# Optimization experiments

Hardware: AMD Instinct MI355X
Metric: run time of the kernel (lower is better)

## Reference

```python
import jax, jax.numpy as jnp
import numpy as np

N_NODES = 50000
N_EDGES = 800000
D_FEAT = 128
D_HID = 500


def setup_inputs() -> dict:
    key = jax.random.key(0)
    k1, k2, k3, k4 = jax.random.split(key, 4)
    x = jax.random.normal(k1, (N_NODES, D_FEAT), dtype=jnp.float32)
    edge_index = jax.random.randint(k2, (2, N_EDGES), 0, N_NODES, dtype=jnp.int64)
    # Glorot-ish init for weights, zeros for bias (PyG GCNConv default)
    W1 = jax.random.normal(k3, (D_FEAT, D_HID), dtype=jnp.float32) / np.sqrt(D_FEAT)
    b1 = jnp.zeros((D_HID,), dtype=jnp.float32)
    W2 = jax.random.normal(k4, (D_HID, 1), dtype=jnp.float32) / np.sqrt(D_HID)
    b2 = jnp.zeros((1,), dtype=jnp.float32)
    return {"x": x, "edge_index": edge_index, "W1": W1, "b1": b1, "W2": W2, "b2": b2}


def gcn_conv(x, W, b, src, dst, n_nodes):
    """PyG GCNConv: linear transform, add self-loops, symmetric norm, scatter-add, bias."""
    h = x @ W  # [N, out]
    loops = jnp.arange(n_nodes, dtype=src.dtype)
    s = jnp.concatenate([src, loops])  # [E+N]
    d = jnp.concatenate([dst, loops])
    deg = jnp.zeros((n_nodes,), dtype=h.dtype).at[d].add(1.0)
    dinv = jnp.where(deg > 0, jax.lax.rsqrt(deg), 0.0)
    norm = dinv[s] * dinv[d]  # [E+N]
    msg = h[s] * norm[:, None]  # [E+N, out] -- dominant memory traffic
    out = jax.ops.segment_sum(msg, d, num_segments=n_nodes)
    return out + b


def reference(x, edge_index, W1, b1, W2, b2):
    src, dst = edge_index[0], edge_index[1]
    n = x.shape[0]
    h = gcn_conv(x, W1, b1, src, dst, n)
    h = jax.nn.relu(h)
    # F.dropout(training=self.training): identity in eval mode
    out = gcn_conv(h, W2, b2, src, dst, n)
    return out
```

## Files before the change

### kernel.cpp

```cpp
#include <hip/hip_runtime.h>


#define N_NODES 50000
#define N_EDGES 800000
#define D_FEAT  128
#define D_HID   500
#define NTILES  3125
#define RB      782
#define CSTRIDE 64

typedef __bf16 bf16x8 __attribute__((ext_vector_type(8)));
typedef float  f32x4  __attribute__((ext_vector_type(4)));

static __device__ inline unsigned int f2bf(float f) {
    unsigned int u = __float_as_uint(f);
    return (u + 0x7fffu + ((u >> 16) & 1u)) >> 16;
}
static __device__ inline float bf_lo(unsigned int u) { return __uint_as_float(u << 16); }
static __device__ inline float bf_hi(unsigned int u) { return __uint_as_float(u & 0xffff0000u); }

static __device__ inline void add8(float* acc, uint4 u) {
    acc[0] += bf_lo(u.x);
    acc[1] += bf_hi(u.x);
    acc[2] += bf_lo(u.y);
    acc[3] += bf_hi(u.y);
    acc[4] += bf_lo(u.z);
    acc[5] += bf_hi(u.z);
    acc[6] += bf_lo(u.w);
    acc[7] += bf_hi(u.w);
}

__global__ __launch_bounds__(256) void k_rank(const int* __restrict__ dst,
                                              const float* __restrict__ W1,
                                              const float* __restrict__ b1,
                                              const float* __restrict__ W2,
                                              int* __restrict__ deg,
                                              int* __restrict__ rank,
                                              unsigned short* __restrict__ b_pk,
                                              float* __restrict__ b1p,
                                              float* __restrict__ w2p) {
    const int b = blockIdx.x, tid = threadIdx.x;
    if (b < RB) {
        int t4 = b * 256 + tid;
        if (t4 < N_EDGES / 4) {
            int e = t4 * 4;
            int4 d4 = *(const int4*)&dst[e];
            int4 r4;
            r4.x = atomicAdd(&deg[d4.x], 1);
            r4.y = atomicAdd(&deg[d4.y], 1);
            r4.z = atomicAdd(&deg[d4.z], 1);
            r4.w = atomicAdd(&deg[d4.w], 1);
            *(int4*)&rank[e] = r4;
        }
    } else if (b < RB + 32) {
        int idx  = (b - RB) * 256 + tid;
        int lane = idx & 63;
        int slot = idx >> 6;
        int t    = slot >> 2;
        int ks   = slot & 3;
        int quad = lane >> 4;
        int n    = t * 16 + (lane & 15);
        unsigned int us[8];
#pragma unroll
        for (int j = 0; j < 8; j++) {
            int k = ks * 32 + quad * 8 + j;
            float v = (n < D_HID) ? W1[(size_t)k * D_HID + n] : 0.f;
            us[j] = f2bf(v);
        }
        uint4 p;
        p.x = us[0] | (us[1] << 16);
        p.y = us[2] | (us[3] << 16);
        p.z = us[4] | (us[5] << 16);
        p.w = us[6] | (us[7] << 16);
        ((uint4*)b_pk)[idx] = p;
    } else {
        for (int i = tid; i < 512; i += 256) {
            b1p[i] = (i < D_HID) ? b1[i] : 0.f;
            w2p[i] = (i < D_HID) ? W2[i] : 0.f;
        }
    }
}

__global__ __launch_bounds__(256) void k_fill(const int* __restrict__ src,
                                              const int* __restrict__ dst,
                                              const int* __restrict__ rank,
                                              const int* __restrict__ deg,
                                              const float* __restrict__ x,
                                              int* __restrict__ csrp,
                                              uint2* __restrict__ xd) {
    const int e = blockIdx.x * 256 + threadIdx.x;
    {
        int r = rank[e];
        if (r < CSTRIDE)
            csrp[dst[e] * CSTRIDE + r] = src[e];
    }
    for (int i = e; i < N_NODES * D_FEAT / 4; i += N_EDGES) {
        float d = rsqrtf((float)(deg[i >> 5] + 1));
        float4 v = ((const float4*)x)[i];
        uint2 o;
        o.x = f2bf(d * v.x) | (f2bf(d * v.y) << 16);
        o.y = f2bf(d * v.z) | (f2bf(d * v.w) << 16);
        xd[i] = o;
    }
}

__global__ __launch_bounds__(256, 4) void k_gcn1(const uint4* __restrict__ xd4,
                                                 const int* __restrict__ csrp,
                                                 const int* __restrict__ deg,
                                                 const unsigned short* __restrict__ b_pk,
                                                 const float* __restrict__ b1p,
                                                 const float* __restrict__ w2p,
                                                 float* __restrict__ zd) {
    __shared__ unsigned short A[16][136];
    __shared__ float red[4][16];
    const int t = threadIdx.x;
    const int node0 = blockIdx.x * 16;
    const int wv = t >> 6, lane = t & 63;
    const int q = lane >> 4, p = lane & 15;

    {
        const int n = wv * 4 + q;
        const int node = node0 + n;
        int dg = deg[node];
        if (dg > CSTRIDE) dg = CSTRIDE;
        const int base = node * CSTRIDE;
        float acc[8];
#pragma unroll
        for (int j = 0; j < 8; j++) acc[j] = 0.f;

        int e = 0;
        for (; e + 4 <= dg; e += 4) {
            int4 s4 = *(const int4*)&csrp[base + e];
            uint4 u0 = xd4[(size_t)s4.x * 16 + p];
            uint4 u1 = xd4[(size_t)s4.y * 16 + p];
            uint4 u2 = xd4[(size_t)s4.z * 16 + p];
            uint4 u3 = xd4[(size_t)s4.w * 16 + p];
            add8(acc, u0);
            add8(acc, u1);
            add8(acc, u2);
            add8(acc, u3);
        }
        for (; e < dg; e++) {
            int s = csrp[base + e];
            uint4 u = xd4[(size_t)s * 16 + p];
            add8(acc, u);
        }

        const float di = rsqrtf((float)(dg + 1));
        uint4 su = xd4[(size_t)node * 16 + p];
        uint4 o;
        o.x = f2bf(di * (acc[0] + bf_lo(su.x))) |
              (f2bf(di * (acc[1] + bf_hi(su.x))) << 16);
        o.y = f2bf(di * (acc[2] + bf_lo(su.y))) |
              (f2bf(di * (acc[3] + bf_hi(su.y))) << 16);
        o.z = f2bf(di * (acc[4] + bf_lo(su.z))) |
              (f2bf(di * (acc[5] + bf_hi(su.z))) << 16);
        o.w = f2bf(di * (acc[6] + bf_lo(su.w))) |
              (f2bf(di * (acc[7] + bf_hi(su.w))) << 16);
        *(uint4*)&A[n][p * 8] = o;
    }
    __syncthreads();

    bf16x8 afr[4];
#pragma unroll
    for (int ks = 0; ks < 4; ks++)
        afr[ks] = *(const bf16x8*)&A[p][ks * 32 + q * 8];

    const bf16x8* __restrict__ bpk = (const bf16x8*)b_pk;
    f32x4 acc[8];
#pragma unroll
    for (int tt = 0; tt < 8; tt++) acc[tt] = (f32x4){0.f, 0.f, 0.f, 0.f};
#pragma unroll
    for (int tt = 0; tt < 8; tt++) {
        const int tile_n = wv * 8 + tt;
#pragma unroll
        for (int ks = 0; ks < 4; ks++) {
            bf16x8 bfr = bpk[(size_t)(tile_n * 4 + ks) * 64 + lane];
            acc[tt] = __builtin_amdgcn_mfma_f32_16x16x32_bf16(afr[ks], bfr, acc[tt], 0, 0, 0);
        }
    }

    float zp[4] = {0.f, 0.f, 0.f, 0.f};
#pragma unroll
    for (int tt = 0; tt < 8; tt++) {
        const int c = (wv * 8 + tt) * 16 + p;
        const float b1v = b1p[c];
        const float w2v = w2p[c];
#pragma unroll
        for (int r = 0; r < 4; r++)
            zp[r] += fmaxf(acc[tt][r] + b1v, 0.f) * w2v;
    }
#pragma unroll
    for (int off = 1; off < 16; off <<= 1) {
#pragma unroll
        for (int r = 0; r < 4; r++) zp[r] += __shfl_xor(zp[r], off);
    }
    if (p == 0) {
#pragma unroll
        for (int r = 0; r < 4; r++) red[wv][q * 4 + r] = zp[r];
    }
    __syncthreads();
    if (t < 16) {
        int node = node0 + t;
        float zz = red[0][t] + red[1][t] + red[2][t] + red[3][t];
        zd[node] = rsqrtf((float)(deg[node] + 1)) * zz;
    }
}

__global__ __launch_bounds__(256) void k_gz(const int* __restrict__ csrp,
                                            const int* __restrict__ deg,
                                            const float* __restrict__ zd,
                                            const float* __restrict__ b2,
                                            float* __restrict__ out) {
    const int node = blockIdx.x * 16 + (threadIdx.x >> 4);
    const int l = threadIdx.x & 15;
    int dg = deg[node];
    if (dg > CSTRIDE) dg = CSTRIDE;
    const int base = node * CSTRIDE;
    float s = 0.f;
    for (int e = l; e < dg; e += 16) s += zd[csrp[base + e]];
#pragma unroll
    for (int off = 1; off < 16; off <<= 1) s += __shfl_xor(s, off);
    if (l == 0) {
        float di = rsqrtf((float)(dg + 1));
        out[node] = di * (s + zd[node]) + b2[0];
    }
}

extern "C" void kernel_launch(void* const* d_in, const int* in_sizes, int n_in,
                              void* d_out, int out_size, void* d_ws, size_t ws_size,
                              hipStream_t stream) {
    const float* x  = (const float*)d_in[0];
    const int*   ei = (const int*)d_in[1];
    const float* W1 = (const float*)d_in[2];
    const float* b1 = (const float*)d_in[3];
    const float* W2 = (const float*)d_in[4];
    const float* b2 = (const float*)d_in[5];
    float* out = (float*)d_out;

    const int* src = ei;
    const int* dst = ei + N_EDGES;

    uint2* xd            = (uint2*)d_ws;
    unsigned short* b_pk = (unsigned short*)(xd + 1600000);
    float* b1p    = (float*)(b_pk + 65536);
    float* w2p    = b1p + 512;
    float* zd     = w2p + 512;
    int* deg      = (int*)(zd + N_NODES);
    int* rank     = deg + N_NODES;
    int* csrp     = rank + N_EDGES;

    hipMemsetAsync(deg, 0, N_NODES * sizeof(int), stream);

    k_rank<<<RB + 33, 256, 0, stream>>>(dst, W1, b1, W2, deg, rank, b_pk, b1p, w2p);
    k_fill<<<NTILES, 256, 0, stream>>>(src, dst, rank, deg, x, csrp, xd);
    k_gcn1<<<NTILES, 256, 0, stream>>>((const uint4*)xd, csrp, deg,
                                       b_pk, b1p, w2p, zd);
    k_gz  <<<NTILES, 256, 0, stream>>>(csrp, deg, zd, b2, out);
}
```

Baseline: 183.7 us.

## Move x bf16 conversion into rank kernel and apply source norm in gather

The x-to-bf16 conversion no longer depends on degrees, so it moves into the first kernel and runs alongside the degree atomics. The source-side normalisation becomes a per-edge deg lookup and rsqrt inside the layer-1 gather, using fma. The fill kernel now only scatters CSR entries, four edges per thread with vector loads. In exchange, the gather kernel does one extra random deg load per edge and loses the pre-scaled features.

```diff
diff --git a/kernel.cpp b/kernel.cpp
--- a/kernel.cpp
+++ b/kernel.cpp
@@ -7,6 +7,7 @@
 #define D_HID   500
 #define NTILES  3125
 #define RB      782
+#define XB      1563
 #define CSTRIDE 64
 
 typedef __bf16 bf16x8 __attribute__((ext_vector_type(8)));
@@ -19,23 +20,25 @@
 static __device__ inline float bf_lo(unsigned int u) { return __uint_as_float(u << 16); }
 static __device__ inline float bf_hi(unsigned int u) { return __uint_as_float(u & 0xffff0000u); }
 
-static __device__ inline void add8(float* acc, uint4 u) {
-    acc[0] += bf_lo(u.x);
-    acc[1] += bf_hi(u.x);
-    acc[2] += bf_lo(u.y);
-    acc[3] += bf_hi(u.y);
-    acc[4] += bf_lo(u.z);
-    acc[5] += bf_hi(u.z);
-    acc[6] += bf_lo(u.w);
-    acc[7] += bf_hi(u.w);
+static __device__ inline void fma8(float* acc, uint4 u, float w) {
+    acc[0] = fmaf(w, bf_lo(u.x), acc[0]);
+    acc[1] = fmaf(w, bf_hi(u.x), acc[1]);
+    acc[2] = fmaf(w, bf_lo(u.y), acc[2]);
+    acc[3] = fmaf(w, bf_hi(u.y), acc[3]);
+    acc[4] = fmaf(w, bf_lo(u.z), acc[4]);
+    acc[5] = fmaf(w, bf_hi(u.z), acc[5]);
+    acc[6] = fmaf(w, bf_lo(u.w), acc[6]);
+    acc[7] = fmaf(w, bf_hi(u.w), acc[7]);
 }
 
 __global__ __launch_bounds__(256) void k_rank(const int* __restrict__ dst,
+                                              const float* __restrict__ x,
                                               const float* __restrict__ W1,
                                               const float* __restrict__ b1,
                                               const float* __restrict__ W2,
                                               int* __restrict__ deg,
                                               int* __restrict__ rank,
+                                              uint2* __restrict__ xb,
                                               unsigned short* __restrict__ b_pk,
                                               float* __restrict__ b1p,
                                               float* __restrict__ w2p) {
@@ -52,8 +55,21 @@
             r4.w = atomicAdd(&deg[d4.w], 1);
             *(int4*)&rank[e] = r4;
         }
-    } else if (b < RB + 32) {
-        int idx  = (b - RB) * 256 + tid;
+    } else if (b < RB + XB) {
+        const int base = (b - RB) * 1024;
+#pragma unroll
+        for (int j = 0; j < 4; j++) {
+            int i = base + j * 256 + tid;
+            if (i < N_NODES * D_FEAT / 4) {
+                float4 v = ((const float4*)x)[i];
+                uint2 o;
+                o.x = f2bf(v.x) | (f2bf(v.y) << 16);
+                o.y = f2bf(v.z) | (f2bf(v.w) << 16);
+                xb[i] = o;
+            }
+        }
+    } else if (b < RB + XB + 32) {
+        int idx  = (b - RB - XB) * 256 + tid;
         int lane = idx & 63;
         int slot = idx >> 6;
         int t    = slot >> 2;
@@ -84,27 +100,20 @@
 __global__ __launch_bounds__(256) void k_fill(const int* __restrict__ src,
                                               const int* __restrict__ dst,
                                               const int* __restrict__ rank,
-                                              const int* __restrict__ deg,
-                                              const float* __restrict__ x,
-                                              int* __restrict__ csrp,
-                                              uint2* __restrict__ xd) {
-    const int e = blockIdx.x * 256 + threadIdx.x;
-    {
-        int r = rank[e];
-        if (r < CSTRIDE)
-            csrp[dst[e] * CSTRIDE + r] = src[e];
-    }
-    for (int i = e; i < N_NODES * D_FEAT / 4; i += N_EDGES) {
-        float d = rsqrtf((float)(deg[i >> 5] + 1));
-        float4 v = ((const float4*)x)[i];
-        uint2 o;
-        o.x = f2bf(d * v.x) | (f2bf(d * v.y) << 16);
-        o.y = f2bf(d * v.z) | (f2bf(d * v.w) << 16);
-        xd[i] = o;
-    }
-}
-
-__global__ __launch_bounds__(256, 4) void k_gcn1(const uint4* __restrict__ xd4,
+                                              int* __restrict__ csrp) {
+    int t4 = blockIdx.x * 256 + threadIdx.x;
+    if (t4 >= N_EDGES / 4) return;
+    int e = t4 * 4;
+    int4 s4 = *(const int4*)&src[e];
+    int4 d4 = *(const int4*)&dst[e];
+    int4 r4 = *(const int4*)&rank[e];
+    if (r4.x < CSTRIDE) csrp[d4.x * CSTRIDE + r4.x] = s4.x;
+    if (r4.y < CSTRIDE) csrp[d4.y * CSTRIDE + r4.y] = s4.y;
+    if (r4.z < CSTRIDE) csrp[d4.z * CSTRIDE + r4.z] = s4.z;
+    if (r4.w < CSTRIDE) csrp[d4.w * CSTRIDE + r4.w] = s4.w;
+}
+
+__global__ __launch_bounds__(256, 4) void k_gcn1(const uint4* __restrict__ xb4,
                                                  const int* __restrict__ csrp,
                                                  const int* __restrict__ deg,
                                                  const unsigned short* __restrict__ b_pk,
@@ -131,32 +140,34 @@
         int e = 0;
         for (; e + 4 <= dg; e += 4) {
             int4 s4 = *(const int4*)&csrp[base + e];
-            uint4 u0 = xd4[(size_t)s4.x * 16 + p];
-            uint4 u1 = xd4[(size_t)s4.y * 16 + p];
-            uint4 u2 = xd4[(size_t)s4.z * 16 + p];
-            uint4 u3 = xd4[(size_t)s4.w * 16 + p];
-            add8(acc, u0);
-            add8(acc, u1);
-            add8(acc, u2);
-            add8(acc, u3);
+            int g0 = deg[s4.x], g1 = deg[s4.y], g2 = deg[s4.z], g3 = deg[s4.w];
+            uint4 u0 = xb4[(size_t)s4.x * 16 + p];
+            uint4 u1 = xb4[(size_t)s4.y * 16 + p];
+            uint4 u2 = xb4[(size_t)s4.z * 16 + p];
+            uint4 u3 = xb4[(size_t)s4.w * 16 + p];
+            fma8(acc, u0, rsqrtf((float)(g0 + 1)));
+            fma8(acc, u1, rsqrtf((float)(g1 + 1)));
+            fma8(acc, u2, rsqrtf((float)(g2 + 1)));
+            fma8(acc, u3, rsqrtf((float)(g3 + 1)));
         }
         for (; e < dg; e++) {
             int s = csrp[base + e];
-            uint4 u = xd4[(size_t)s * 16 + p];
-            add8(acc, u);
+            int g = deg[s];
+            uint4 u = xb4[(size_t)s * 16 + p];
+            fma8(acc, u, rsqrtf((float)(g + 1)));
         }
 
         const float di = rsqrtf((float)(dg + 1));
-        uint4 su = xd4[(size_t)node * 16 + p];
+        uint4 su = xb4[(size_t)node * 16 + p];
         uint4 o;
-        o.x = f2bf(di * (acc[0] + bf_lo(su.x))) |
-              (f2bf(di * (acc[1] + bf_hi(su.x))) << 16);
-        o.y = f2bf(di * (acc[2] + bf_lo(su.y))) |
-              (f2bf(di * (acc[3] + bf_hi(su.y))) << 16);
-        o.z = f2bf(di * (acc[4] + bf_lo(su.z))) |
-              (f2bf(di * (acc[5] + bf_hi(su.z))) << 16);
-        o.w = f2bf(di * (acc[6] + bf_lo(su.w))) |
-              (f2bf(di * (acc[7] + bf_hi(su.w))) << 16);
+        o.x = f2bf(di * (acc[0] + di * bf_lo(su.x))) |
+              (f2bf(di * (acc[1] + di * bf_hi(su.x))) << 16);
+        o.y = f2bf(di * (acc[2] + di * bf_lo(su.y))) |
+              (f2bf(di * (acc[3] + di * bf_hi(su.y))) << 16);
+        o.z = f2bf(di * (acc[4] + di * bf_lo(su.z))) |
+              (f2bf(di * (acc[5] + di * bf_hi(su.z))) << 16);
+        o.w = f2bf(di * (acc[6] + di * bf_lo(su.w))) |
+              (f2bf(di * (acc[7] + di * bf_hi(su.w))) << 16);
         *(uint4*)&A[n][p * 8] = o;
     }
     __syncthreads();
@@ -241,8 +252,8 @@
     const int* src = ei;
     const int* dst = ei + N_EDGES;
 
-    uint2* xd            = (uint2*)d_ws;
-    unsigned short* b_pk = (unsigned short*)(xd + 1600000);
+    uint2* xb            = (uint2*)d_ws;
+    unsigned short* b_pk = (unsigned short*)(xb + 1600000);
     float* b1p    = (float*)(b_pk + 65536);
     float* w2p    = b1p + 512;
     float* zd     = w2p + 512;
@@ -252,9 +263,10 @@
 
     hipMemsetAsync(deg, 0, N_NODES * sizeof(int), stream);
 
-    k_rank<<<RB + 33, 256, 0, stream>>>(dst, W1, b1, W2, deg, rank, b_pk, b1p, w2p);
-    k_fill<<<NTILES, 256, 0, stream>>>(src, dst, rank, deg, x, csrp, xd);
-    k_gcn1<<<NTILES, 256, 0, stream>>>((const uint4*)xd, csrp, deg,
+    k_rank<<<RB + XB + 33, 256, 0, stream>>>(dst, x, W1, b1, W2, deg, rank,
+                                             xb, b_pk, b1p, w2p);
+    k_fill<<<RB, 256, 0, stream>>>(src, dst, rank, csrp);
+    k_gcn1<<<NTILES, 256, 0, stream>>>((const uint4*)xb, csrp, deg,
                                        b_pk, b1p, w2p, zd);
     k_gz  <<<NTILES, 256, 0, stream>>>(csrp, deg, zd, b2, out);
 }
```

Result: faster. 178.9 us (-2.6%).
